# Kernel optimization log

Hardware: AMD Instinct MI355X
Metric: run time of the kernel (lower is better)

The kernel has to match this reference:

```python
import jax, jax.numpy as jnp
import numpy as np

V0, V1, V2 = 8000, 4000, 4096   # diag / proc / med vocab sizes
E = 512                          # emb_dim
T, L = 64, 48                    # visits, codes per visit
FAI = 0.05                       # history-selection threshold
EPS = 1e-5                       # LayerNorm eps (torch default)

def _normalize(adj):
    # GCN.normalize: row-normalize (adj + I)
    adj = adj + np.eye(adj.shape[0], dtype=np.float64)
    rowsum = adj.sum(1)
    r_inv = np.where(rowsum > 0, 1.0 / rowsum, 0.0)
    return (r_inv[:, None] * adj).astype(np.float32)

def setup_inputs() -> dict:
    key = jax.random.key(0)
    ks = iter(jax.random.split(key, 48))
    p = lambda *s: jax.random.normal(next(ks), s, jnp.float32) * 0.02
    rng = np.random.default_rng(0)
    def rand_adj():
        a = rng.random((V2, V2)) < 0.01
        a = (a | a.T).astype(np.float64)
        np.fill_diagonal(a, 0.0)
        return a
    ehr = rand_adj(); ddi = rand_adj()
    return dict(
        diag_codes=jax.random.randint(next(ks), (T, L), 0, V0),
        proc_codes=jax.random.randint(next(ks), (T, L), 0, V1),
        emb0=p(V0, E), emb1=p(V1, E), emb2=p(V2, E),
        gru1_Wih=p(3 * E, E), gru1_Whh=p(3 * E, E), gru1_bih=p(3 * E), gru1_bhh=p(3 * E),
        gru2_Wih=p(3 * E, E), gru2_Whh=p(3 * E, E), gru2_bih=p(3 * E), gru2_bhh=p(3 * E),
        query_W=p(E, 2 * E), query_b=p(E),
        poly_h1_W=p(32, 2 * E), poly_h1_b=p(32), poly_gate_W=p(1, 32), poly_gate_b=p(1),
        cls_W=p(V2, 2 * E), cls_b=p(V2),
        ln_gamma=jnp.ones((E,), jnp.float32), ln_beta=jnp.zeros((E,), jnp.float32),
        ehr_W1=p(V2, E), ehr_b1=p(E), ehr_W2=p(E, E), ehr_b2=p(E),
        ddi_W1=p(V2, E), ddi_b1=p(E), ddi_W2=p(E, E), ddi_b2=p(E),
        inter1=p(1),
        ehr_adj_norm=jnp.asarray(_normalize(ehr)),
        ddi_adj_norm=jnp.asarray(_normalize(ddi)),
        ddi_adj=jnp.asarray(ddi.astype(np.float32)),
    )

def _gru_last(x_seq, mask, Wih, Whh, bih, bhh):
    # torch nn.GRU cell, batch=1; masked-out steps carry h unchanged, which
    # equals running the GRU over only the selected subsequence. Only the
    # final hidden state is needed (original uses output[-1]).
    def step(h, inp):
        x, m = inp
        gi = x @ Wih.T + bih          # [3E]
        gh = h @ Whh.T + bhh
        ir, iz, inn = jnp.split(gi, 3)
        hr, hz, hn = jnp.split(gh, 3)
        r = jax.nn.sigmoid(ir + hr)
        z = jax.nn.sigmoid(iz + hz)
        n = jnp.tanh(inn + r * hn)
        h_new = (1.0 - z) * n + z * h
        return jnp.where(m, h_new, h), None
    h0 = jnp.zeros((Wih.shape[1],), x_seq.dtype)
    h_final, _ = jax.lax.scan(step, h0, (x_seq, mask))
    return h_final

def reference(diag_codes, proc_codes, emb0, emb1, emb2,
              gru1_Wih, gru1_Whh, gru1_bih, gru1_bhh,
              gru2_Wih, gru2_Whh, gru2_bih, gru2_bhh,
              query_W, query_b, poly_h1_W, poly_h1_b, poly_gate_W, poly_gate_b,
              cls_W, cls_b, ln_gamma, ln_beta,
              ehr_W1, ehr_b1, ehr_W2, ehr_b2, ddi_W1, ddi_b1, ddi_W2, ddi_b2,
              inter1, ehr_adj_norm, ddi_adj_norm, ddi_adj):
    i1 = emb0[diag_codes].sum(1)            # [T,E] per-visit sum pooling
    i2 = emb1[proc_codes].sum(1)            # [T,E]
    rep = jnp.concatenate([i1, i2], -1)     # [T,2E] patient representation
    # Aggregation gate for history selection
    hidden = jax.nn.relu(rep @ poly_h1_W.T + poly_h1_b)
    gate = jax.nn.sigmoid(hidden @ poly_gate_W.T + poly_gate_b)[:, 0]  # [T]
    s = jnp.abs(gate[-1] - gate[:-1])
    mask = jnp.concatenate([s <= FAI, jnp.ones((1,), bool)])  # last visit always kept
    h1 = _gru_last(i1, mask, gru1_Wih, gru1_Whh, gru1_bih, gru1_bhh)
    h2 = _gru_last(i2, mask, gru2_Wih, gru2_Whh, gru2_bih, gru2_bhh)
    q_in = jnp.concatenate([h1, h2])                      # [2E]
    query = (jax.nn.relu(q_in) @ query_W.T + query_b)[None, :]  # [1,E]
    def gcn(W1, b1, W2, b2, adj):
        h = jax.nn.relu(adj @ W1 + b1)    # x = I so x@W1 = W1 (dropout eval)
        return adj @ (h @ W2) + b2
    safe = gcn(ehr_W1, ehr_b1, ehr_W2, ehr_b2, ehr_adj_norm) \
         - inter1 * gcn(ddi_W1, ddi_b1, ddi_W2, ddi_b2, ddi_adj_norm)
    drug = safe + emb2                                    # [V2,E]
    kw = jax.nn.softmax(query @ drug.T, -1)               # [1,V2]
    med = kw @ drug                                       # [1,E]
    mu = query.mean(-1, keepdims=True)
    var = ((query - mu) ** 2).mean(-1, keepdims=True)
    ln = (query - mu) / jnp.sqrt(var + EPS) * ln_gamma + ln_beta
    final = jnp.concatenate([ln, med], -1)                # [1,2E]
    result = jax.nn.relu(final) @ cls_W.T + cls_b         # [1,V2]
    neg = jax.nn.sigmoid(result)
    batch_neg = 0.0005 * ((neg.T * neg) * ddi_adj).sum()
    return result, batch_neg
```

## Files before the change

### kernel.cpp

```cpp
#include <hip/hip_runtime.h>
#include <cstdint>
#include <cstddef>

typedef unsigned short u16;
typedef unsigned int   u32;

typedef __bf16 bf16x8 __attribute__((ext_vector_type(8)));
typedef float  f32x4  __attribute__((ext_vector_type(4)));

__device__ __forceinline__ float uAsF(u32 u){ union{u32 u; float f;} c; c.u=u; return c.f; }
__device__ __forceinline__ float b2f(u16 v){ return uAsF(((u32)v)<<16); }
__device__ __forceinline__ u16 f2b(float f){
  union{float f; u32 u;} c; c.f=f; u32 x=c.u;
  u32 r = (x + 0x7fffu + ((x>>16)&1u)) >> 16;
  return (u16)r;
}
__device__ __forceinline__ void unpack8(uint4 p, float* f){
  f[0]=uAsF(p.x<<16); f[1]=uAsF(p.x&0xffff0000u);
  f[2]=uAsF(p.y<<16); f[3]=uAsF(p.y&0xffff0000u);
  f[4]=uAsF(p.z<<16); f[5]=uAsF(p.z&0xffff0000u);
  f[6]=uAsF(p.w<<16); f[7]=uAsF(p.w&0xffff0000u);
}
__device__ __forceinline__ float sigm(float x){ return 1.f/(1.f+__expf(-x)); }

// ... 25 lines not shown
}
__device__ __forceinline__ uint4 ld8p(const void* p, size_t i, int f32){
  if (f32){
    const float4* q = (const float4*)((const float*)p + i);
    float4 a = q[0], b = q[1];
    uint4 r;
    r.x = (u32)f2b(a.x) | ((u32)f2b(a.y)<<16);
    r.y = (u32)f2b(a.z) | ((u32)f2b(a.w)<<16);
    r.z = (u32)f2b(b.x) | ((u32)f2b(b.y)<<16);
    r.w = (u32)f2b(b.z) | ((u32)f2b(b.w)<<16);
    return r;
  }
  return *(const uint4*)((const u16*)p + i);
}

constexpr size_t OFF_I1    = 0;
constexpr size_t OFF_I2    = 0x20000;
constexpr size_t OFF_GI    = 0x40000;
constexpr size_t OFF_GATE  = 0x100000;
constexpr size_t OFF_HBUF  = 0x100800;
constexpr size_t OFF_HFIN  = 0x102800;
constexpr size_t OFF_CTR   = 0x103800;
constexpr size_t OFF_NEGA  = 0x103900;
constexpr size_t OFF_QUERY = 0x104000;
constexpr size_t OFF_SE    = 0x105000;
constexpr size_t OFF_SD    = 0x109000;
constexpr size_t OFF_SEMB  = 0x10D000;
constexpr size_t OFF_KW    = 0x111000;
constexpr size_t OFF_U     = 0x115000;
constexpr size_t OFF_Y     = 0x119000;
constexpr size_t OFF_Z     = 0x11D000;
constexpr size_t OFF_ME    = 0x11D800;
constexpr size_t OFF_MD    = 0x11E000;
constexpr size_t OFF_MEMB  = 0x11E800;
constexpr size_t OFF_FIN   = 0x11F000;
constexpr size_t OFF_NEG   = 0x120000;
constexpr size_t OFF_W1T   = 0x124000;
constexpr size_t OFF_H     = 0x524000;
// ... 7 lines not shown

constexpr size_t OFF_UD    = OFF_GI + 0x0000;
constexpr size_t OFF_Y2    = OFF_GI + 0x4000;
constexpr size_t OFF_Z2    = OFF_GI + 0x8000;
constexpr size_t OFF_WVD   = OFF_GI + 0x8800;
constexpr size_t OFF_WVE   = OFF_GI + 0x9000;

__global__ __launch_bounds__(256) void k_cvt(const void* __restrict__ S, u16* __restrict__ D,
                                             const u16* __restrict__ dt)
{
  int f32 = dprobe(dt);
  size_t i8 = ((size_t)blockIdx.x*256 + threadIdx.x) * 8;
  *(uint4*)(D + i8) = ld8p(S, i8, f32);
}

__global__ __launch_bounds__(256) void k_gather(const int* __restrict__ dc, const int* __restrict__ pc,
    const void* __restrict__ emb0, const void* __restrict__ emb1,
    float* __restrict__ i1, float* __restrict__ i2, const u16* __restrict__ dt)
{
  int f32 = dprobe(dt);
  int t = blockIdx.x;
  int which = blockIdx.y;
  const int* codes = which ? pc : dc;
  const void* emb  = which ? emb1 : emb0;
  float* out       = which ? i2 : i1;
  int e = threadIdx.x;
  float s0=0.f, s1=0.f;
  for (int l=0;l<48;l++){
    int c = codes[t*48+l];
    size_t base = (size_t)c*512;
    s0 += ld1(emb, base+e, f32);
    s1 += ld1(emb, base+e+256, f32);
  }
  out[t*512+e] = s0;
  out[t*512+e+256] = s1;
}

__global__ __launch_bounds__(256) void k_gate(const float* __restrict__ i1, const float* __restrict__ i2,
    const void* __restrict__ phW, const void* __restrict__ phb,
    const void* __restrict__ pgW, const void* __restrict__ pgb,
    float* __restrict__ gate, const u16* __restrict__ dt)
{
  int f32 = dprobe(dt);
  int t = blockIdx.x;
  __shared__ float rep[1024];
  __shared__ float hid[32];
  int tid = threadIdx.x;
  for (int q=0;q<4;q++){
    int k = tid + q*256;
    rep[k] = (k<512) ? i1[t*512+k] : i2[t*512+k-512];
  }
  __syncthreads();
  int w = tid>>6, lane = tid&63;
  for (int jj=0;jj<8;jj++){
    int j = w*8 + jj;
    float s = 0.f;
    for (int k=lane;k<1024;k+=64) s += rep[k]*ld1(phW, (size_t)j*1024+k, f32);
    for (int off=32;off;off>>=1) s += __shfl_down(s, off);
    if (lane==0) hid[j] = fmaxf(s + ld1(phb, j, f32), 0.f);
  }
  __syncthreads();
  if (tid==0){
    float s = 0.f;
    for (int j=0;j<32;j++) s += hid[j]*ld1(pgW, j, f32);
    gate[t] = sigm(s + ld1(pgb, 0, f32));
  }
}

__global__ __launch_bounds__(256) void k_gi(const void* __restrict__ Wih0, const void* __restrict__ Wih1,
    const void* __restrict__ bih0, const void* __restrict__ bih1,
    const float* __restrict__ i1, const float* __restrict__ i2,
    float* __restrict__ gi, const u16* __restrict__ dt)
{
  int f32 = dprobe(dt);
  int g  = blockIdx.y;
  int t0 = blockIdx.x*4;
  const void* W   = g ? Wih1 : Wih0;
  const void* bih = g ? bih1 : bih0;
  const float* x = g ? i2 : i1;
  __shared__ float xl[4*512];
  int tid = threadIdx.x;
  for (int q=0;q<8;q++) xl[tid + q*256] = x[t0*512 + tid + q*256];
  __syncthreads();
  int j = blockIdx.z*256 + tid;
  float b = ld1(bih, j, f32);
  float a0=0.f,a1=0.f,a2=0.f,a3=0.f;
  for (int k=0;k<512;k+=8){
    float f[8]; ld8(W, (size_t)j*512 + k, f32, f);
    #pragma unroll
    for (int xx=0;xx<8;xx++){
      float wv = f[xx];
      a0 += wv*xl[k+xx];
      a1 += wv*xl[512+k+xx];
      a2 += wv*xl[1024+k+xx];
      a3 += wv*xl[1536+k+xx];
    }
  }
  float* og = gi + (size_t)g*64*1536;
  og[(size_t)(t0+0)*1536 + j] = a0 + b;
  og[(size_t)(t0+1)*1536 + j] = a1 + b;
  og[(size_t)(t0+2)*1536 + j] = a2 + b;
  og[(size_t)(t0+3)*1536 + j] = a3 + b;
}

__global__ __launch_bounds__(512, 2) void k_gruf(
    const void* __restrict__ Whh0, const void* __restrict__ Whh1,
    const void* __restrict__ bhh0, const void* __restrict__ bhh1,
    const float* __restrict__ gi, const float* __restrict__ gate,
    u32* __restrict__ hbuf, float* __restrict__ hfin, const u16* __restrict__ dt,
    const void* __restrict__ trS, u16* __restrict__ trD,
    const void* __restrict__ cv0S, u16* __restrict__ cv0D, int nc0,
    const void* __restrict__ cv1S, u16* __restrict__ cv1D, int nc1)
{
  int f32 = dprobe(dt);
  const int tid = threadIdx.x;
  int rb = (int)blockIdx.x - 16;
  if (rb >= 0){
    if (rb < 2048){
      __shared__ u16 tile[32][33];
      int bx = rb & 15, by = rb >> 4;
      int lx = tid & 31, ly = tid >> 5;
      int c = bx*32 + lx;
      #pragma unroll
      for (int i=0;i<2;i++){
        int r = by*32 + ly + i*16;
        size_t idx = (size_t)r*512 + c;
        tile[ly+i*16][lx] = f32 ? f2b(((const float*)trS)[idx]) : ((const u16*)trS)[idx];
      }
      __syncthreads();
      int r2 = by*32 + lx;
      #pragma unroll
      for (int i=0;i<2;i++){
// ... 50 lines not shown
    } else {
      const uint4* src = (const uint4*)((const u16*)Whh + base);
      #pragma unroll
      for (int q=0;q<4;q++){
        uint4 pk = src[q];
        wreg[i*16+q*4+0]=pk.x; wreg[i*16+q*4+1]=pk.y;
        wreg[i*16+q*4+2]=pk.z; wreg[i*16+q*4+3]=pk.w;
      }
    }
  }
  if (tid < 64) gl[tid] = gate[tid];
  h_lds[tid] = 0.f;
  __syncthreads();
  if (tid < 64)
    mask_l[tid] = (tid==63) ? 1 : (fabsf(gl[63] - gl[tid]) <= 0.05f ? 1 : 0);
  __syncthreads();

  int s = 0;
  for (int t=0;t<64;t++){
    if (!mask_l[t]) continue;
    s++;
    const int p = s & 1;
    float acc6[6] = {0.f,0.f,0.f,0.f,0.f,0.f};
    const float2* h2 = ((const float2*)h_lds) + cg*16;
    #pragma unroll
    for (int q=0;q<16;q++){
      float2 hv = h2[q];
      #pragma unroll
      for (int i=0;i<6;i++){
        u32 wp = wreg[i*16+q];
// ... 51 lines not shown
  #pragma unroll
  for (int i=0;i<4;i++){
    int r = blockIdx.y*32 + ly + i*8;
    size_t idx = (size_t)r*C + c;
    tile[ly+i*8][lx] = f32 ? f2b(((const float*)S)[idx]) : ((const u16*)S)[idx];
  }
  __syncthreads();
  int r2 = blockIdx.y*32 + lx;
  #pragma unroll
  for (int i=0;i<4;i++){
    int c2 = blockIdx.x*32 + ly + i*8;
    D[(size_t)c2*R + r2] = tile[lx][ly+i*8];
  }
}

__global__ __launch_bounds__(256)
void k_gemm(const void* __restrict__ A, const u16* __restrict__ Bt,
            const void* __restrict__ bias, u16* __restrict__ C, int K,
            const u16* __restrict__ adt, const u16* __restrict__ bdt)
{
  int af32 = dprobe(adt), bf32 = dprobe(bdt);
  const int m0 = blockIdx.x * 64;
  const int n0 = blockIdx.y * 128;
  const int tid = threadIdx.x;
  const int lane = tid & 63;
  const int wv = tid >> 6;
  const int wr = wv >> 1, wc = wv & 1;
  const int l15 = lane & 15, lq = lane >> 4;

  __shared__ u16 As[2][64*64];
  __shared__ u16 Bs[2][128*64];

  f32x4 acc[2][4];
  #pragma unroll
  for (int i=0;i<2;i++)
    #pragma unroll
    for (int j=0;j<4;j++)
      acc[i][j] = (f32x4){0.f,0.f,0.f,0.f};

  const int srow = tid >> 3;
  const int sc8  = tid & 7;
  const size_t grow_a = (size_t)(m0 + srow) * K + sc8*8;
  const size_t grow_b = (size_t)(n0 + srow) * K + sc8*8;
  const int adst0 = srow*64 + ((sc8 ^ (srow&7))*8);
  const int adst1 = (32+srow)*64 + ((sc8 ^ ((32+srow)&7))*8);
  int bdst[4];
  #pragma unroll
  for (int q=0;q<4;q++){
    int row = q*32 + srow;
    bdst[q] = row*64 + ((sc8 ^ (row&7))*8);
  }

  {
    uint4 va0 = ld8p(A, grow_a, af32);
    uint4 va1 = ld8p(A, grow_a + (size_t)32*K, af32);
    uint4 vb[4];
    #pragma unroll
    for (int q=0;q<4;q++) vb[q] = *(const uint4*)(Bt + grow_b + (size_t)q*32*K);
    *(uint4*)(As[0] + adst0) = va0;
    *(uint4*)(As[0] + adst1) = va1;
    #pragma unroll
    for (int q=0;q<4;q++) *(uint4*)(Bs[0] + bdst[q]) = vb[q];
  }
  __syncthreads();

  for (int k0 = 0; k0 < K; k0 += 64){
    const int cur = (k0 >> 6) & 1;
    const int nxt = 1 - cur;
    uint4 va0, va1, vb[4];
    const bool more = (k0 + 64) < K;
    if (more){
      va0 = ld8p(A, grow_a + k0 + 64, af32);
      va1 = ld8p(A, grow_a + (size_t)32*K + k0 + 64, af32);
      #pragma unroll
      for (int q=0;q<4;q++) vb[q] = *(const uint4*)(Bt + grow_b + (size_t)q*32*K + k0 + 64);
    }
    #pragma unroll
    for (int ks=0; ks<2; ++ks){
      bf16x8 af[2], bfr[4];
      #pragma unroll
      for (int i=0;i<2;i++){
        int ar = wr*32 + i*16 + l15;
        af[i]  = *(const bf16x8*)(As[cur] + ar*64 + (((ks*4+lq) ^ (ar&7))*8));
      }
      #pragma unroll
      for (int j=0;j<4;j++){
        int br = wc*64 + j*16 + l15;
        bfr[j] = *(const bf16x8*)(Bs[cur] + br*64 + (((ks*4+lq) ^ (br&7))*8));
      }
      #pragma unroll
      for (int i=0;i<2;i++)
        #pragma unroll
        for (int j=0;j<4;j++)
          acc[i][j] = __builtin_amdgcn_mfma_f32_16x16x32_bf16(af[i], bfr[j], acc[i][j], 0,0,0);
    }
    if (more){
      *(uint4*)(As[nxt] + adst0) = va0;
      *(uint4*)(As[nxt] + adst1) = va1;
      #pragma unroll
      for (int q=0;q<4;q++) *(uint4*)(Bs[nxt] + bdst[q]) = vb[q];
      __syncthreads();
    }
  }

  #pragma unroll
  for (int i=0;i<2;i++){
    int row = wr*32 + i*16 + lq*4;
    #pragma unroll
    for (int j=0;j<4;j++){
      int col = wc*64 + j*16 + l15;
      int n = n0 + col;
      float bv = ld1(bias, n, bf32);
      #pragma unroll
      for (int r=0;r<4;r++){
        float v = fmaxf(acc[i][j][r] + bv, 0.f);
        C[(size_t)(m0+row+r)*512 + n] = f2b(v);
      }
    }
  }
}

__global__ __launch_bounds__(256) void k_matvec(const void* __restrict__ A, const float* __restrict__ x,
    float* __restrict__ y, int M, int Kc, const u16* __restrict__ dt)
{
  int f32 = dprobe(dt);
  __shared__ float xl[4096];
  int tid = threadIdx.x;
  for (int k=tid; k<Kc; k+=256) xl[k] = x[k];
  __syncthreads();
  int w = tid>>6, lane = tid&63;
  int r0 = blockIdx.x*16 + w*4;
  for (int i=0;i<4;i++){
    int r = r0 + i;
    float s = 0.f;
    for (int k0 = lane*8; k0 < Kc; k0 += 512){
      float f[8]; ld8(A, (size_t)r*Kc + k0, f32, f);
      #pragma unroll
      for (int xx=0;xx<8;xx++) s += f[xx]*xl[k0+xx];
    }
    for (int off=32;off;off>>=1) s += __shfl_down(s, off);
    if (lane==0) y[r] = s;
  }
}

__global__ __launch_bounds__(256) void k_mvp(
    const void* __restrict__ A0, const float* __restrict__ x0, float* __restrict__ y0, const u16* d0,
    const void* __restrict__ A1, const float* __restrict__ x1, float* __restrict__ y1, const u16* d1,
    int Kc, int half)
{
  __shared__ float xl[4096];
  int bx = blockIdx.x, tid = threadIdx.x;
  const void* A; const float* x; float* y; const u16* dtp; int xb;
  if (bx < half){ A=A0; x=x0; y=y0; dtp=d0; xb=bx; }
  else          { A=A1; x=x1; y=y1; dtp=d1; xb=bx-half; }
  int f32 = dprobe(dtp);
  for (int k=tid; k<Kc; k+=256) xl[k] = x[k];
  __syncthreads();
  int w = tid>>6, lane = tid&63;
  int r0 = xb*16 + w*4;
  for (int i=0;i<4;i++){
    int r = r0 + i;
    float s = 0.f;
    for (int k0 = lane*8; k0 < Kc; k0 += 512){
      float f[8]; ld8(A, (size_t)r*Kc + k0, f32, f);
      #pragma unroll
      for (int xx=0;xx<8;xx++) s += f[xx]*xl[k0+xx];
    }
    for (int off=32;off;off>>=1) s += __shfl_down(s, off);
    if (lane==0) y[r] = s;
  }
}

__global__ __launch_bounds__(256) void k_colreduce(const void* __restrict__ A, const float* __restrict__ w,
    float* __restrict__ y, int C, const u16* __restrict__ dt)
{
  int f32 = dprobe(dt);
  __shared__ float wl[256];
  int tid = threadIdx.x;
  int v0 = blockIdx.y*256;
  wl[tid] = w[v0+tid];
  __syncthreads();
  int k = blockIdx.x*256 + tid;
  float acc = 0.f;
  size_t base = (size_t)v0*C + k;
  for (int i=0;i<256;i++) acc += wl[i]*ld1(A, base + (size_t)i*C, f32);
  atomicAdd(&y[k], acc);
}

__global__ __launch_bounds__(256) void k_cr3(
    const void* __restrict__ Ae, const u16* aedt, float* __restrict__ ye,
    const void* __restrict__ Ad, const u16* addt, float* __restrict__ yd,
    const void* __restrict__ E2, const u16* edt, float* __restrict__ ym,
    const float* __restrict__ kw)
{
  __shared__ float wl[256];
  int tid = threadIdx.x, bx = blockIdx.x;
  int v0 = blockIdx.y*256;
  wl[tid] = kw[v0+tid];
  __syncthreads();
  const void* A; float* y; int C, k, f32;
  if (bx < 16){ A=Ae; y=ye; C=4096; k=bx*256+tid; f32=dprobe(aedt); }
  else if (bx < 32){ A=Ad; y=yd; C=4096; k=(bx-16)*256+tid; f32=dprobe(addt); }
  else { A=E2; y=ym; C=512; k=(bx-32)*256+tid; f32=dprobe(edt); }
  float acc = 0.f;
  size_t base = (size_t)v0*C + k;
  for (int i=0;i<256;i++) acc += wl[i]*ld1(A, base + (size_t)i*C, f32);
  atomicAdd(&y[k], acc);
}

__global__ __launch_bounds__(256) void k_crp(
    const void* __restrict__ A0, const float* __restrict__ w0, float* __restrict__ y0, const u16* d0,
    const void* __restrict__ A1, const float* __restrict__ w1, float* __restrict__ y1, const u16* d1,
    int C, int half)
{
  __shared__ float wl[256];
  int tid = threadIdx.x, bx = blockIdx.x;
  int v0 = blockIdx.y*256;
  const void* A; const float* w; float* y; const u16* dtp; int xk;
  if (bx < half){ A=A0; w=w0; y=y0; dtp=d0; xk=bx; }
  else          { A=A1; w=w1; y=y1; dtp=d1; xk=bx-half; }
  int f32 = dprobe(dtp);
  wl[tid] = w[v0+tid];
  __syncthreads();
  int k = xk*256 + tid;
  float acc = 0.f;
  size_t base = (size_t)v0*C + k;
  for (int i=0;i<256;i++) acc += wl[i]*ld1(A, base + (size_t)i*C, f32);
  atomicAdd(&y[k], acc);
}

__global__ void k_zero(float* __restrict__ p, int n){
  int i = blockIdx.x*1024 + threadIdx.x;
  if (i < n) p[i] = 0.f;
}

__global__ __launch_bounds__(256) void k_mv3(
    const void* __restrict__ E2, const void* __restrict__ W2d, const void* __restrict__ W2e,
    const float* __restrict__ query,
    float* __restrict__ s_emb, float* __restrict__ wv_d, float* __restrict__ wv_e,
// ... 158 lines not shown
      float f[4]; ld4(ddi, base + k, f32, f);
      s += f[0]*nl[k] + f[1]*nl[k+1] + f[2]*nl[k+2] + f[3]*nl[k+3];
    }
    for (int off=32;off;off>>=1) s += __shfl_down(s, off);
    if (lane==0) tot += nl[ii]*s;
  }
  if (lane==0) atomicAdd(acc, tot);
  __syncthreads();
  if (tid == 0){
    __threadfence();
    u32 old = atomicAdd(ctr, 1u);
    if (old == (u32)(gridDim.x - 1)){
      float v = 0.0005f * __hip_atomic_load(acc, __ATOMIC_RELAXED, __HIP_MEMORY_SCOPE_AGENT);
      if (f32) ((float*)outv)[4096] = v; else ((u16*)outv)[4096] = f2b(v);
    }
  }
}

__global__ void k_diag(u16* __restrict__ outv, float dv)
{
  int i = blockIdx.x*256 + threadIdx.x;
  if (i <= 4096) outv[i] = (i==0) ? f2b(dv) : (u16)0;
}

extern "C" void kernel_launch(void* const* d_in, const int* in_sizes, int n_in,
                              void* d_out, int out_size, void* d_ws, size_t ws_size,
                              hipStream_t stream)
{
  (void)in_sizes; (void)n_in; (void)out_size;
  const int* diag = (const int*)d_in[0];
// ... 31 lines not shown

  const bool hasHd  = ws_size >= NEED_C2;
  const bool hasAb  = ws_size >= NEED_B;
  const bool hasAb2 = ws_size >= NEED_A;
  const bool mergedTail = hasHd && (hasAb2 || !hasAb);

  char* ws = (char*)d_ws;
  float* i1    = (float*)(ws + OFF_I1);
  float* i2    = (float*)(ws + OFF_I2);
  float* gi    = (float*)(ws + OFF_GI);
  float* gate  = (float*)(ws + OFF_GATE);
  u32*   hbuf  = (u32*)  (ws + OFF_HBUF);
  float* hfin  = (float*)(ws + OFF_HFIN);
  u32*   ctr   = (u32*)  (ws + OFF_CTR);
  float* nega  = (float*)(ws + OFF_NEGA);
  float* query = (float*)(ws + OFF_QUERY);
  float* s_e   = (float*)(ws + OFF_SE);
  float* s_d   = (float*)(ws + OFF_SD);
  float* s_emb = (float*)(ws + OFF_SEMB);
  float* kw    = (float*)(ws + OFF_KW);
  float* u_e   = (float*)(ws + OFF_U);
  float* y     = (float*)(ws + OFF_Y);
  float* z     = (float*)(ws + OFF_Z);
  float* me    = (float*)(ws + OFF_ME);
  float* md    = (float*)(ws + OFF_MD);
  float* memb  = (float*)(ws + OFF_MEMB);
  float* fin   = (float*)(ws + OFF_FIN);
  float* neg   = (float*)(ws + OFF_NEG);
  u16*   W1T   = (u16*)  (ws + OFF_W1T);
  u16*   h     = (u16*)  (ws + OFF_H);
  u16*   h_d   = hasHd ? (u16*)(ws + OFF_HD) : h;
  u16*   AbD   = (u16*)  (ws + OFF_ABD);
  u16*   AbE   = hasAb2 ? (u16*)(ws + OFF_ABE) : AbD;
  float* u_d   = (float*)(ws + OFF_UD);
  float* y2    = (float*)(ws + OFF_Y2);
  float* z2    = (float*)(ws + OFF_Z2);
  float* wv_d  = (float*)(ws + OFF_WVD);
  float* wv_e  = (float*)(ws + OFF_WVE);
  void*  outv  = d_out;

  const void* Ad   = hasAb ? (const void*)AbD : dAdjN;
  const u16*  adt  = hasAb ? (const u16*)nullptr : dt;
  const void* Ae   = hasAb ? (const void*)AbE : eAdj;
  const u16*  aedt = hasAb ? (const u16*)nullptr : dt;

  k_gather<<<dim3(64,2), 256, 0, stream>>>(diag, proc, emb0, emb1, i1, i2, dt);
  k_gate<<<64, 256, 0, stream>>>(i1, i2, phW, phb, pgW, pgb, gate, dt);
  k_gi<<<dim3(16,2,6), 256, 0, stream>>>(g1Wih, g2Wih, g1bih, g2bih, i1, i2, gi, dt);

  {
    int nc0 = hasAb  ? 4096 : 0;
    int nc1 = hasAb2 ? 4096 : 0;
    k_gruf<<<16 + 2048 + nc0 + nc1, 512, 0, stream>>>(
        g1Whh, g2Whh, g1bhh, g2bhh, gi, gate, hbuf, hfin, dt,
        dW1, W1T,
        dAdjN, AbD, nc0,
        eAdj,  AbE, nc1);
  }
  k_query<<<8, 256, 0, stream>>>(hfin, qW, qb, query, dt);
  k_mv3<<<328, 256, 0, stream>>>(emb2, dW2, eW2, query, s_emb, wv_d, wv_e,
                                 y, y2, nega, ctr, dt);

  if (mergedTail){
    k_gemm<<<dim3(64,4), 256, 0, stream>>>(Ad, W1T, db1, h_d, 4096, adt, dt);
    k_transpose<<<dim3(16,128), 256, 0, stream>>>(eW1, W1T, 4096, 512, dt);
    k_gemm<<<dim3(64,4), 256, 0, stream>>>(Ae, W1T, eb1, h, 4096, aedt, dt);
    k_mvp<<<512, 256, 0, stream>>>(h, wv_e, u_e, nullptr, h_d, wv_d, u_d, nullptr, 512, 256);
    k_mvp<<<512, 256, 0, stream>>>(Ae, u_e, s_e, aedt, Ad, u_d, s_d, adt, 4096, 256);
    k_softmax<<<1, 1024, 0, stream>>>(s_e, s_d, s_emb, inter1, kw, dt);
    k_cr3<<<dim3(34,16), 256, 0, stream>>>(Ae, aedt, y, Ad, adt, y2, emb2, dt, memb, kw);
    k_crp<<<dim3(4,16), 256, 0, stream>>>(h, y, z, nullptr, h_d, y2, z2, nullptr, 512, 2);
    k_crp<<<dim3(4,2), 256, 0, stream>>>(eW2, z, me, dt, dW2, z2, md, dt, 512, 2);
  } else {
    k_gemm<<<dim3(64,4), 256, 0, stream>>>(Ad, W1T, db1, h_d, 4096, adt, dt);
    k_matvec<<<256, 256, 0, stream>>>(h_d, wv_d, u_e, 4096, 512, nullptr);
    k_matvec<<<256, 256, 0, stream>>>(Ad, u_e, s_d, 4096, 4096, adt);

    if (hasAb) k_cvt<<<8192, 256, 0, stream>>>(eAdj, AbE, dt);
    k_transpose<<<dim3(16,128), 256, 0, stream>>>(eW1, W1T, 4096, 512, dt);
    k_gemm<<<dim3(64,4), 256, 0, stream>>>(Ae, W1T, eb1, h, 4096, aedt, dt);
    k_matvec<<<256, 256, 0, stream>>>(h, wv_e, u_e, 4096, 512, nullptr);
    k_matvec<<<256, 256, 0, stream>>>(Ae, u_e, s_e, 4096, 4096, aedt);

    k_softmax<<<1, 1024, 0, stream>>>(s_e, s_d, s_emb, inter1, kw, dt);

    k_colreduce<<<dim3(16,16), 256, 0, stream>>>(Ae, kw, y, 4096, aedt);
    k_colreduce<<<dim3(2,16),  256, 0, stream>>>(h,  y,  z, 512,  nullptr);
    k_colreduce<<<dim3(2,2),   256, 0, stream>>>(eW2, z, me, 512, dt);
    k_colreduce<<<dim3(2,16),  256, 0, stream>>>(emb2, kw, memb, 512, dt);

    k_zero<<<5, 1024, 0, stream>>>(y, 4608);
    if (hasAb && !hasAb2) k_cvt<<<8192, 256, 0, stream>>>(dAdjN, AbD, dt);
    if (!hasHd){
      k_transpose<<<dim3(16,128), 256, 0, stream>>>(dW1, W1T, 4096, 512, dt);
      k_gemm<<<dim3(64,4), 256, 0, stream>>>(Ad, W1T, db1, h, 4096, adt, dt);
    }
    k_colreduce<<<dim3(16,16), 256, 0, stream>>>(Ad, kw, y, 4096, adt);
    k_colreduce<<<dim3(2,16),  256, 0, stream>>>(h_d, y, z, 512, nullptr);
    k_colreduce<<<dim3(2,2),   256, 0, stream>>>(dW2, z, md, 512, dt);
  }

  k_ln<<<1, 512, 0, stream>>>(query, me, md, memb, eb2, db2, inter1, lng, lnb, fin, dt);
  k_cls<<<64, 256, 0, stream>>>(fin, clsW, clsb, outv, neg, dt);
  k_negsum<<<128, 256, 0, stream>>>(dAdj, neg, nega, ctr, outv, dt);
}
```

Measured before the change: 1.067 ms.

## Fuse tail into persistent kernel with grid barriers; merge gather/gate and gi into GRU launch

Replaces the chain of about a dozen tail launches (query, matvecs, two GEMMs, softmax, column reductions, layernorm, classifier, negsum) with one persistent 256-block kernel that separates phases using atomic-counter grid barriers. Gather and gate become one kernel, and the input-projection GEMM runs as extra blocks inside the GRU launch, which spin-waits on a counter before starting the recurrence. The goal is to remove launch gaps and small-kernel tails. The cost is spin-barrier overhead, GEMMs limited to 256 resident blocks, and a deadlock risk if not all blocks are co-resident.

```diff
diff --git a/kernel.cpp b/kernel.cpp
--- a/kernel.cpp
+++ b/kernel.cpp
@@ -63,6 +63,18 @@
   return *(const uint4*)((const u16*)p + i);
 }
 
+__device__ __forceinline__ void gbar(u32* cell, u32 n){
+  __syncthreads();
+  if (threadIdx.x == 0){
+    __threadfence();
+    __hip_atomic_fetch_add(cell, 1u, __ATOMIC_RELEASE, __HIP_MEMORY_SCOPE_AGENT);
+    while (__hip_atomic_load(cell, __ATOMIC_ACQUIRE, __HIP_MEMORY_SCOPE_AGENT) < n)
+      __builtin_amdgcn_s_sleep(2);
+    __threadfence();
+  }
+  __syncthreads();
+}
+
 constexpr size_t OFF_I1    = 0;
 constexpr size_t OFF_I2    = 0x20000;
 constexpr size_t OFF_GI    = 0x40000;
@@ -71,6 +83,7 @@
 constexpr size_t OFF_HFIN  = 0x102800;
 constexpr size_t OFF_CTR   = 0x103800;
 constexpr size_t OFF_NEGA  = 0x103900;
+constexpr size_t OFF_BAR   = 0x103A00;
 constexpr size_t OFF_QUERY = 0x104000;
 constexpr size_t OFF_SE    = 0x105000;
 constexpr size_t OFF_SD    = 0x109000;
@@ -108,42 +121,36 @@
   *(uint4*)(D + i8) = ld8p(S, i8, f32);
 }
 
-__global__ __launch_bounds__(256) void k_gather(const int* __restrict__ dc, const int* __restrict__ pc,
+__global__ __launch_bounds__(256) void k_gg(const int* __restrict__ dc, const int* __restrict__ pc,
     const void* __restrict__ emb0, const void* __restrict__ emb1,
-    float* __restrict__ i1, float* __restrict__ i2, const u16* __restrict__ dt)
-{
-  int f32 = dprobe(dt);
-  int t = blockIdx.x;
-  int which = blockIdx.y;
-  const int* codes = which ? pc : dc;
-  const void* emb  = which ? emb1 : emb0;
-  float* out       = which ? i2 : i1;
-  int e = threadIdx.x;
-  float s0=0.f, s1=0.f;
-  for (int l=0;l<48;l++){
-    int c = codes[t*48+l];
-    size_t base = (size_t)c*512;
-    s0 += ld1(emb, base+e, f32);
-    s1 += ld1(emb, base+e+256, f32);
-  }
-  out[t*512+e] = s0;
-  out[t*512+e+256] = s1;
-}
-
-__global__ __launch_bounds__(256) void k_gate(const float* __restrict__ i1, const float* __restrict__ i2,
     const void* __restrict__ phW, const void* __restrict__ phb,
     const void* __restrict__ pgW, const void* __restrict__ pgb,
-    float* __restrict__ gate, const u16* __restrict__ dt)
-{
+    float* __restrict__ i1, float* __restrict__ i2, float* __restrict__ gate,
+    u32* __restrict__ bars, float* __restrict__ nega, const u16* __restrict__ dt)
+{
+  int tid = threadIdx.x;
+  if (blockIdx.x == 64){
+    if (tid < 32) bars[tid] = 0u;
+    if (tid == 32) *nega = 0.f;
+    return;
+  }
   int f32 = dprobe(dt);
   int t = blockIdx.x;
   __shared__ float rep[1024];
   __shared__ float hid[32];
-  int tid = threadIdx.x;
-  for (int q=0;q<4;q++){
-    int k = tid + q*256;
-    rep[k] = (k<512) ? i1[t*512+k] : i2[t*512+k-512];
-  }
+  float s0=0.f, s1=0.f, s2=0.f, s3=0.f;
+  for (int l=0;l<48;l++){
+    int c0 = dc[t*48+l];
+    int c1 = pc[t*48+l];
+    size_t b0 = (size_t)c0*512, b1 = (size_t)c1*512;
+    s0 += ld1(emb0, b0+tid, f32);
+    s1 += ld1(emb0, b0+tid+256, f32);
+    s2 += ld1(emb1, b1+tid, f32);
+    s3 += ld1(emb1, b1+tid+256, f32);
+  }
+  i1[t*512+tid] = s0; i1[t*512+tid+256] = s1;
+  i2[t*512+tid] = s2; i2[t*512+tid+256] = s3;
+  rep[tid] = s0; rep[tid+256] = s1; rep[512+tid] = s2; rep[768+tid] = s3;
   __syncthreads();
   int w = tid>>6, lane = tid&63;
   for (int jj=0;jj<8;jj++){
@@ -161,47 +168,15 @@
   }
 }
 
-__global__ __launch_bounds__(256) void k_gi(const void* __restrict__ Wih0, const void* __restrict__ Wih1,
+__global__ __launch_bounds__(512, 2) void k_gruf2(
+    const void* __restrict__ Whh0, const void* __restrict__ Whh1,
+    const void* __restrict__ bhh0, const void* __restrict__ bhh1,
+    const void* __restrict__ Wih0, const void* __restrict__ Wih1,
     const void* __restrict__ bih0, const void* __restrict__ bih1,
     const float* __restrict__ i1, const float* __restrict__ i2,
-    float* __restrict__ gi, const u16* __restrict__ dt)
-{
-  int f32 = dprobe(dt);
-  int g  = blockIdx.y;
-  int t0 = blockIdx.x*4;
-  const void* W   = g ? Wih1 : Wih0;
-  const void* bih = g ? bih1 : bih0;
-  const float* x = g ? i2 : i1;
-  __shared__ float xl[4*512];
-  int tid = threadIdx.x;
-  for (int q=0;q<8;q++) xl[tid + q*256] = x[t0*512 + tid + q*256];
-  __syncthreads();
-  int j = blockIdx.z*256 + tid;
-  float b = ld1(bih, j, f32);
-  float a0=0.f,a1=0.f,a2=0.f,a3=0.f;
-  for (int k=0;k<512;k+=8){
-    float f[8]; ld8(W, (size_t)j*512 + k, f32, f);
-    #pragma unroll
-    for (int xx=0;xx<8;xx++){
-      float wv = f[xx];
-      a0 += wv*xl[k+xx];
-      a1 += wv*xl[512+k+xx];
-      a2 += wv*xl[1024+k+xx];
-      a3 += wv*xl[1536+k+xx];
-    }
-  }
-  float* og = gi + (size_t)g*64*1536;
-  og[(size_t)(t0+0)*1536 + j] = a0 + b;
-  og[(size_t)(t0+1)*1536 + j] = a1 + b;
-  og[(size_t)(t0+2)*1536 + j] = a2 + b;
-  og[(size_t)(t0+3)*1536 + j] = a3 + b;
-}
-
-__global__ __launch_bounds__(512, 2) void k_gruf(
-    const void* __restrict__ Whh0, const void* __restrict__ Whh1,
-    const void* __restrict__ bhh0, const void* __restrict__ bhh1,
-    const float* __restrict__ gi, const float* __restrict__ gate,
-    u32* __restrict__ hbuf, float* __restrict__ hfin, const u16* __restrict__ dt,
+    float* __restrict__ gi, const float* __restrict__ gate,
+    u32* __restrict__ hbuf, float* __restrict__ hfin,
+    u32* __restrict__ bars, const u16* __restrict__ dt,
     const void* __restrict__ trS, u16* __restrict__ trD,
     const void* __restrict__ cv0S, u16* __restrict__ cv0D, int nc0,
     const void* __restrict__ cv1S, u16* __restrict__ cv1D, int nc1)
@@ -210,6 +185,41 @@
   const int tid = threadIdx.x;
   int rb = (int)blockIdx.x - 16;
   if (rb >= 0){
+    if (rb < 96){
+      __shared__ float xg[2048];
+      int g = (rb>>4)&1, z = rb>>5, t0 = (rb&15)*4;
+      const float* x   = g ? i2 : i1;
+      const void* W    = g ? Wih1 : Wih0;
+      const void* bih  = g ? bih1 : bih0;
+      for (int q=0;q<4;q++) xg[tid + q*512] = x[t0*512 + tid + q*512];
+      __syncthreads();
+      int j = z*512 + tid;
+      float b = ld1(bih, j, f32);
+      float a0=0.f,a1=0.f,a2=0.f,a3=0.f;
+      for (int k=0;k<512;k+=8){
+        float f[8]; ld8(W, (size_t)j*512 + k, f32, f);
+        #pragma unroll
+        for (int xx=0;xx<8;xx++){
+          float wv = f[xx];
+          a0 += wv*xg[k+xx];
+          a1 += wv*xg[512+k+xx];
+          a2 += wv*xg[1024+k+xx];
+          a3 += wv*xg[1536+k+xx];
+        }
+      }
+      float* og = gi + (size_t)g*64*1536;
+      og[(size_t)(t0+0)*1536 + j] = a0 + b;
+      og[(size_t)(t0+1)*1536 + j] = a1 + b;
+      og[(size_t)(t0+2)*1536 + j] = a2 + b;
+      og[(size_t)(t0+3)*1536 + j] = a3 + b;
+      __syncthreads();
+      if (tid == 0){
+        __threadfence();
+        __hip_atomic_fetch_add(&bars[31], 1u, __ATOMIC_RELEASE, __HIP_MEMORY_SCOPE_AGENT);
+      }
+      return;
+    }
+    rb -= 96;
     if (rb < 2048){
       __shared__ u16 tile[32][33];
       int bx = rb & 15, by = rb >> 4;
@@ -290,6 +300,12 @@
   __syncthreads();
   if (tid < 64)
     mask_l[tid] = (tid==63) ? 1 : (fabsf(gl[63] - gl[tid]) <= 0.05f ? 1 : 0);
+  __syncthreads();
+  if (tid == 0){
+    while (__hip_atomic_load(&bars[31], __ATOMIC_ACQUIRE, __HIP_MEMORY_SCOPE_AGENT) < 96u)
+      __builtin_amdgcn_s_sleep(2);
+    __threadfence();
+  }
   __syncthreads();
 
   int s = 0;
@@ -371,22 +387,16 @@
   }
 }
 
-__global__ __launch_bounds__(256)
-void k_gemm(const void* __restrict__ A, const u16* __restrict__ Bt,
-            const void* __restrict__ bias, u16* __restrict__ C, int K,
-            const u16* __restrict__ adt, const u16* __restrict__ bdt)
-{
-  int af32 = dprobe(adt), bf32 = dprobe(bdt);
-  const int m0 = blockIdx.x * 64;
-  const int n0 = blockIdx.y * 128;
-  const int tid = threadIdx.x;
+__device__ __forceinline__ void gemm_body(const void* A, const u16* Bt,
+    const void* bias, u16* C, int af32, int bf32, int task, u16* As, u16* Bs, int tid)
+{
+  const int K = 4096;
+  const int m0 = (task & 63) * 64;
+  const int n0 = (task >> 6) * 128;
   const int lane = tid & 63;
   const int wv = tid >> 6;
   const int wr = wv >> 1, wc = wv & 1;
   const int l15 = lane & 15, lq = lane >> 4;
-
-  __shared__ u16 As[2][64*64];
-  __shared__ u16 Bs[2][128*64];
 
   f32x4 acc[2][4];
   #pragma unroll
@@ -414,10 +424,10 @@
     uint4 vb[4];
     #pragma unroll
     for (int q=0;q<4;q++) vb[q] = *(const uint4*)(Bt + grow_b + (size_t)q*32*K);
-    *(uint4*)(As[0] + adst0) = va0;
-    *(uint4*)(As[0] + adst1) = va1;
+    *(uint4*)(As + adst0) = va0;
+    *(uint4*)(As + adst1) = va1;
     #pragma unroll
-    for (int q=0;q<4;q++) *(uint4*)(Bs[0] + bdst[q]) = vb[q];
+    for (int q=0;q<4;q++) *(uint4*)(Bs + bdst[q]) = vb[q];
   }
   __syncthreads();
 
@@ -432,18 +442,20 @@
       #pragma unroll
       for (int q=0;q<4;q++) vb[q] = *(const uint4*)(Bt + grow_b + (size_t)q*32*K + k0 + 64);
     }
+    u16* Asc = As + cur*4096;
+    u16* Bsc = Bs + cur*8192;
     #pragma unroll
     for (int ks=0; ks<2; ++ks){
       bf16x8 af[2], bfr[4];
       #pragma unroll
       for (int i=0;i<2;i++){
         int ar = wr*32 + i*16 + l15;
-        af[i]  = *(const bf16x8*)(As[cur] + ar*64 + (((ks*4+lq) ^ (ar&7))*8));
+        af[i]  = *(const bf16x8*)(Asc + ar*64 + (((ks*4+lq) ^ (ar&7))*8));
       }
       #pragma unroll
       for (int j=0;j<4;j++){
         int br = wc*64 + j*16 + l15;
-        bfr[j] = *(const bf16x8*)(Bs[cur] + br*64 + (((ks*4+lq) ^ (br&7))*8));
+        bfr[j] = *(const bf16x8*)(Bsc + br*64 + (((ks*4+lq) ^ (br&7))*8));
       }
       #pragma unroll
       for (int i=0;i<2;i++)
@@ -452,10 +464,12 @@
           acc[i][j] = __builtin_amdgcn_mfma_f32_16x16x32_bf16(af[i], bfr[j], acc[i][j], 0,0,0);
     }
     if (more){
-      *(uint4*)(As[nxt] + adst0) = va0;
-      *(uint4*)(As[nxt] + adst1) = va1;
-      #pragma unroll
-      for (int q=0;q<4;q++) *(uint4*)(Bs[nxt] + bdst[q]) = vb[q];
+      u16* Asn = As + nxt*4096;
+      u16* Bsn = Bs + nxt*8192;
+      *(uint4*)(Asn + adst0) = va0;
+      *(uint4*)(Asn + adst1) = va1;
+      #pragma unroll
+      for (int q=0;q<4;q++) *(uint4*)(Bsn + bdst[q]) = vb[q];
       __syncthreads();
     }
   }
@@ -477,6 +491,19 @@
   }
 }
 
+__global__ __launch_bounds__(256)
+void k_gemm(const void* __restrict__ A, const u16* __restrict__ Bt,
+            const void* __restrict__ bias, u16* __restrict__ C, int K,
+            const u16* __restrict__ adt, const u16* __restrict__ bdt)
+{
+  (void)K;
+  __shared__ __attribute__((aligned(16))) char smem[49152];
+  int task = (int)(blockIdx.x + blockIdx.y*64);
+  int t = (int)blockIdx.x | ((int)blockIdx.y << 6);
+  (void)task;
+  gemm_body(A, Bt, bias, C, dprobe(adt), dprobe(bdt), t, (u16*)smem, (u16*)(smem+16384), threadIdx.x);
+}
+
 __global__ __launch_bounds__(256) void k_matvec(const void* __restrict__ A, const float* __restrict__ x,
     float* __restrict__ y, int M, int Kc, const u16* __restrict__ dt)
 {
@@ -500,34 +527,6 @@
   }
 }
 
-__global__ __launch_bounds__(256) void k_mvp(
-    const void* __restrict__ A0, const float* __restrict__ x0, float* __restrict__ y0, const u16* d0,
-    const void* __restrict__ A1, const float* __restrict__ x1, float* __restrict__ y1, const u16* d1,
-    int Kc, int half)
-{
-  __shared__ float xl[4096];
-  int bx = blockIdx.x, tid = threadIdx.x;
-  const void* A; const float* x; float* y; const u16* dtp; int xb;
-  if (bx < half){ A=A0; x=x0; y=y0; dtp=d0; xb=bx; }
-  else          { A=A1; x=x1; y=y1; dtp=d1; xb=bx-half; }
-  int f32 = dprobe(dtp);
-  for (int k=tid; k<Kc; k+=256) xl[k] = x[k];
-  __syncthreads();
-  int w = tid>>6, lane = tid&63;
-  int r0 = xb*16 + w*4;
-  for (int i=0;i<4;i++){
-    int r = r0 + i;
-    float s = 0.f;
-    for (int k0 = lane*8; k0 < Kc; k0 += 512){
-      float f[8]; ld8(A, (size_t)r*Kc + k0, f32, f);
-      #pragma unroll
-      for (int xx=0;xx<8;xx++) s += f[xx]*xl[k0+xx];
-    }
-    for (int off=32;off;off>>=1) s += __shfl_down(s, off);
-    if (lane==0) y[r] = s;
-  }
-}
-
 __global__ __launch_bounds__(256) void k_colreduce(const void* __restrict__ A, const float* __restrict__ w,
     float* __restrict__ y, int C, const u16* __restrict__ dt)
 {
@@ -538,48 +537,6 @@
   wl[tid] = w[v0+tid];
   __syncthreads();
   int k = blockIdx.x*256 + tid;
-  float acc = 0.f;
-  size_t base = (size_t)v0*C + k;
-  for (int i=0;i<256;i++) acc += wl[i]*ld1(A, base + (size_t)i*C, f32);
-  atomicAdd(&y[k], acc);
-}
-
-__global__ __launch_bounds__(256) void k_cr3(
-    const void* __restrict__ Ae, const u16* aedt, float* __restrict__ ye,
-    const void* __restrict__ Ad, const u16* addt, float* __restrict__ yd,
-    const void* __restrict__ E2, const u16* edt, float* __restrict__ ym,
-    const float* __restrict__ kw)
-{
-  __shared__ float wl[256];
-  int tid = threadIdx.x, bx = blockIdx.x;
-  int v0 = blockIdx.y*256;
-  wl[tid] = kw[v0+tid];
-  __syncthreads();
-  const void* A; float* y; int C, k, f32;
-  if (bx < 16){ A=Ae; y=ye; C=4096; k=bx*256+tid; f32=dprobe(aedt); }
-  else if (bx < 32){ A=Ad; y=yd; C=4096; k=(bx-16)*256+tid; f32=dprobe(addt); }
-  else { A=E2; y=ym; C=512; k=(bx-32)*256+tid; f32=dprobe(edt); }
-  float acc = 0.f;
-  size_t base = (size_t)v0*C + k;
-  for (int i=0;i<256;i++) acc += wl[i]*ld1(A, base + (size_t)i*C, f32);
-  atomicAdd(&y[k], acc);
-}
-
-__global__ __launch_bounds__(256) void k_crp(
-    const void* __restrict__ A0, const float* __restrict__ w0, float* __restrict__ y0, const u16* d0,
-    const void* __restrict__ A1, const float* __restrict__ w1, float* __restrict__ y1, const u16* d1,
-    int C, int half)
-{
-  __shared__ float wl[256];
-  int tid = threadIdx.x, bx = blockIdx.x;
-  int v0 = blockIdx.y*256;
-  const void* A; const float* w; float* y; const u16* dtp; int xk;
-  if (bx < half){ A=A0; w=w0; y=y0; dtp=d0; xk=bx; }
-  else          { A=A1; w=w1; y=y1; dtp=d1; xk=bx-half; }
-  int f32 = dprobe(dtp);
-  wl[tid] = w[v0+tid];
-  __syncthreads();
-  int k = xk*256 + tid;
   float acc = 0.f;
   size_t base = (size_t)v0*C + k;
   for (int i=0;i<256;i++) acc += wl[i]*ld1(A, base + (size_t)i*C, f32);
@@ -768,6 +725,317 @@
       float v = 0.0005f * __hip_atomic_load(acc, __ATOMIC_RELAXED, __HIP_MEMORY_SCOPE_AGENT);
       if (f32) ((float*)outv)[4096] = v; else ((u16*)outv)[4096] = f2b(v);
     }
+  }
+}
+
+__global__ __launch_bounds__(256) void k_tail(
+    const float* hfin, const void* qW, const void* qb, float* query,
+    const void* emb2, const void* dW2, const void* eW2,
+    float* s_emb, float* wv_d, float* wv_e,
+    const void* Ad, const u16* adt, const void* Ae, const u16* aedt,
+    u16* W1T, const void* db1, const void* eb1, u16* h_d, u16* h_,
+    const void* eW1,
+    float* u_e, float* u_d, float* s_e, float* s_d,
+    const void* inter1, float* kw,
+    float* y, float* y2, float* z, float* z2,
+    float* me, float* mdp, float* memb,
+    const void* eb2, const void* db2, const void* gam, const void* bet, float* fin,
+    const void* clsW, const void* clsb, void* outv, float* neg,
+    const void* ddi, float* nega, u32* bars, const u16* dt)
+{
+  __shared__ __attribute__((aligned(16))) char smem[49152];
+  float* fsm = (float*)smem;
+  const int tid = threadIdx.x;
+  const int bid = blockIdx.x;
+  const u32 nb = gridDim.x;
+  const int f32 = dprobe(dt);
+  const int af  = dprobe(adt);
+  const int ef  = dprobe(aedt);
+  const int w = tid>>6, lane = tid&63;
+
+  if (bid < 8){
+    float* qin = fsm;
+    for (int q=0;q<4;q++){ int k=tid+q*256; qin[k] = fmaxf(hfin[k], 0.f); }
+    __syncthreads();
+    int row0 = bid*64 + w*16;
+    for (int i=0;i<16;i++){
+      int rr = row0 + i;
+      float s = 0.f;
+      for (int k=lane;k<1024;k+=64) s += qin[k]*ld1(qW, (size_t)rr*1024+k, f32);
+      for (int off=32;off;off>>=1) s += __shfl_down(s, off);
+      if (lane==0) query[rr] = s + ld1(qb, rr, f32);
+    }
+  }
+  gbar(&bars[0], nb);
+
+  {
+    float* xl = fsm;
+    for (int k=tid;k<512;k+=256) xl[k] = query[k];
+    __syncthreads();
+    for (int t=bid; t<327; t+=nb){
+      if (t < 320){
+        const void* A; float* yy; int xb;
+        if (t < 256){ A=emb2; yy=s_emb; xb=t; }
+        else if (t < 288){ A=dW2; yy=wv_d; xb=t-256; }
+        else { A=eW2; yy=wv_e; xb=t-288; }
+        int r0 = xb*16 + w*4;
+        for (int i=0;i<4;i++){
+          int r = r0 + i;
+          float s = 0.f;
+          int k0 = lane*8;
+          float f[8]; ld8(A, (size_t)r*512 + k0, f32, f);
+          #pragma unroll
+          for (int xx=0;xx<8;xx++) s += f[xx]*xl[k0+xx];
+          for (int off=32;off;off>>=1) s += __shfl_down(s, off);
+          if (lane==0) yy[r] = s;
+        }
+      } else if (t < 324){
+        int rb = t - 320;
+        #pragma unroll
+        for (int q=0;q<6;q++){ int i = rb*1536 + q*256 + tid; if (i < 6144) y[i] = 0.f; }
+      } else {
+        int c = t - 324;
+        #pragma unroll
+        for (int q=0;q<6;q++){ int i = c*1536 + q*256 + tid; if (i < 4608) y2[i] = 0.f; }
+      }
+    }
+  }
+  gbar(&bars[1], nb);
+
+  gemm_body(Ad, W1T, db1, h_d, af, f32, bid, (u16*)smem, (u16*)(smem+16384), tid);
+  gbar(&bars[2], nb);
+
+  {
+    u16* tl = (u16*)smem;
+    int lx = tid & 31, ly = tid >> 5;
+    for (int t=bid; t<2048; t+=nb){
+      int bx = t & 15, by = t >> 4;
+      int c = bx*32 + lx;
+      #pragma unroll
+      for (int i=0;i<4;i++){
+        int r = by*32 + ly + i*8;
+        size_t idx = (size_t)r*512 + c;
+        tl[(ly+i*8)*33 + lx] = f32 ? f2b(((const float*)eW1)[idx]) : ((const u16*)eW1)[idx];
+      }
+      __syncthreads();
+      int r2 = by*32 + lx;
+      #pragma unroll
+      for (int i=0;i<4;i++){
+        int c2 = bx*32 + ly + i*8;
+        W1T[(size_t)c2*4096 + r2] = tl[lx*33 + ly+i*8];
+      }
+      __syncthreads();
+    }
+  }
+  gbar(&bars[3], nb);
+
+  gemm_body(Ae, W1T, eb1, h_, ef, f32, bid, (u16*)smem, (u16*)(smem+16384), tid);
+  gbar(&bars[4], nb);
+
+  {
+    float* xl = fsm;
+    for (int t=bid; t<512; t+=nb){
+      const u16* A; const float* x; float* yy; int xb;
+      if (t < 256){ A=h_; x=wv_e; yy=u_e; xb=t; }
+      else { A=h_d; x=wv_d; yy=u_d; xb=t-256; }
+      for (int k=tid;k<512;k+=256) xl[k] = x[k];
+      __syncthreads();
+      int r0 = xb*16 + w*4;
+      for (int i=0;i<4;i++){
+        int r = r0 + i;
+        float s = 0.f;
+        int k0 = lane*8;
+        float f[8]; ld8(A, (size_t)r*512 + k0, 0, f);
+        #pragma unroll
+        for (int xx=0;xx<8;xx++) s += f[xx]*xl[k0+xx];
+        for (int off=32;off;off>>=1) s += __shfl_down(s, off);
+        if (lane==0) yy[r] = s;
+      }
+      __syncthreads();
+    }
+  }
+  gbar(&bars[5], nb);
+
+  {
+    float* xl = fsm;
+    for (int t=bid; t<512; t+=nb){
+      const void* A; const float* x; float* yy; int xb, ff;
+      if (t < 256){ A=Ae; x=u_e; yy=s_e; xb=t; ff=ef; }
+      else { A=Ad; x=u_d; yy=s_d; xb=t-256; ff=af; }
+      for (int k=tid;k<4096;k+=256) xl[k] = x[k];
+      __syncthreads();
+      int r0 = xb*16 + w*4;
+      for (int i=0;i<4;i++){
+        int r = r0 + i;
+        float s = 0.f;
+        for (int k0=lane*8; k0<4096; k0+=512){
+          float f[8]; ld8(A, (size_t)r*4096 + k0, ff, f);
+          #pragma unroll
+          for (int xx=0;xx<8;xx++) s += f[xx]*xl[k0+xx];
+        }
+        for (int off=32;off;off>>=1) s += __shfl_down(s, off);
+        if (lane==0) yy[r] = s;
+      }
+      __syncthreads();
+    }
+  }
+  gbar(&bars[6], nb);
+
+  if (bid == 0){
+    float* red = fsm;
+    float it1 = ld1(inter1, 0, f32);
+    float v[16]; float m = -1e30f;
+    #pragma unroll
+    for (int q=0;q<16;q++){
+      int i = tid + q*256;
+      v[q] = s_e[i] - it1*s_d[i] + s_emb[i];
+      m = fmaxf(m, v[q]);
+    }
+    red[tid] = m; __syncthreads();
+    for (int s=128;s;s>>=1){ if (tid<s) red[tid] = fmaxf(red[tid], red[tid+s]); __syncthreads(); }
+    m = red[0]; __syncthreads();
+    float sum = 0.f;
+    #pragma unroll
+    for (int q=0;q<16;q++){ v[q] = __expf(v[q]-m); sum += v[q]; }
+    red[tid] = sum; __syncthreads();
+    for (int s=128;s;s>>=1){ if (tid<s) red[tid] += red[tid+s]; __syncthreads(); }
+    float inv = 1.f/red[0];
+    #pragma unroll
+    for (int q=0;q<16;q++) kw[tid + q*256] = v[q]*inv;
+  }
+  gbar(&bars[7], nb);
+
+  {
+    float* wl = fsm;
+    for (int t=bid; t<544; t+=nb){
+      int bx = t % 34, by = t / 34;
+      int v0 = by*256;
+      wl[tid] = kw[v0+tid];
+      __syncthreads();
+      const void* A; float* yy; int C, k, ff;
+      if (bx < 16){ A=Ae; yy=y; C=4096; k=bx*256+tid; ff=ef; }
+      else if (bx < 32){ A=Ad; yy=y2; C=4096; k=(bx-16)*256+tid; ff=af; }
+      else { A=emb2; yy=memb; C=512; k=(bx-32)*256+tid; ff=f32; }
+      float acc = 0.f;
+      size_t base = (size_t)v0*C + k;
+      for (int i=0;i<256;i++) acc += wl[i]*ld1(A, base + (size_t)i*C, ff);
+      atomicAdd(&yy[k], acc);
+      __syncthreads();
+    }
+  }
+  gbar(&bars[8], nb);
+
+  {
+    float* wl = fsm;
+    for (int t=bid; t<64; t+=nb){
+      int bx = t & 3, by = t >> 2;
+      int v0 = by*256;
+      const u16* A; const float* ww; float* yy; int xk;
+      if (bx < 2){ A=h_; ww=y; yy=z; xk=bx; }
+      else { A=h_d; ww=y2; yy=z2; xk=bx-2; }
+      wl[tid] = ww[v0+tid];
+      __syncthreads();
+      int k = xk*256 + tid;
+      float acc = 0.f;
+      size_t base = (size_t)v0*512 + k;
+      for (int i=0;i<256;i++) acc += wl[i]*b2f(A[base + (size_t)i*512]);
+      atomicAdd(&yy[k], acc);
+      __syncthreads();
+    }
+  }
+  gbar(&bars[9], nb);
+
+  {
+    float* wl = fsm;
+    for (int t=bid; t<8; t+=nb){
+      int bx = t & 3, by = t >> 2;
+      int v0 = by*256;
+      const void* A; const float* ww; float* yy; int xk;
+      if (bx < 2){ A=eW2; ww=z; yy=me; xk=bx; }
+      else { A=dW2; ww=z2; yy=mdp; xk=bx-2; }
+      wl[tid] = ww[v0+tid];
+      __syncthreads();
+      int k = xk*256 + tid;
+      float acc = 0.f;
+      size_t base = (size_t)v0*512 + k;
+      for (int i=0;i<256;i++) acc += wl[i]*ld1(A, base + (size_t)i*512, f32);
+      atomicAdd(&yy[k], acc);
+      __syncthreads();
+    }
+  }
+  gbar(&bars[10], nb);
+
+  if (bid == 0){
+    float* red = fsm;
+    float q0 = query[tid], q1 = query[tid+256];
+    red[tid] = q0 + q1; __syncthreads();
+    for (int s=128;s;s>>=1){ if (tid<s) red[tid] += red[tid+s]; __syncthreads(); }
+    float mu = red[0]/512.f; __syncthreads();
+    float d0 = q0 - mu, d1 = q1 - mu;
+    red[tid] = d0*d0 + d1*d1; __syncthreads();
+    for (int s=128;s;s>>=1){ if (tid<s) red[tid] += red[tid+s]; __syncthreads(); }
+    float rstd = rsqrtf(red[0]/512.f + 1e-5f);
+    float it1 = ld1(inter1, 0, f32);
+    int e0 = tid, e1 = tid + 256;
+    float ln0 = d0*rstd*ld1(gam,e0,f32) + ld1(bet,e0,f32);
+    float ln1 = d1*rstd*ld1(gam,e1,f32) + ld1(bet,e1,f32);
+    float mv0 = (me[e0] + ld1(eb2,e0,f32)) - it1*(mdp[e0] + ld1(db2,e0,f32)) + memb[e0];
+    float mv1 = (me[e1] + ld1(eb2,e1,f32)) - it1*(mdp[e1] + ld1(db2,e1,f32)) + memb[e1];
+    fin[e0] = fmaxf(ln0, 0.f);
+    fin[e1] = fmaxf(ln1, 0.f);
+    fin[512+e0] = fmaxf(mv0, 0.f);
+    fin[512+e1] = fmaxf(mv1, 0.f);
+  }
+  gbar(&bars[11], nb);
+
+  if (bid < 64){
+    float* fl = fsm;
+    for (int q=0;q<4;q++) fl[tid+q*256] = fin[tid+q*256];
+    __syncthreads();
+    int v0b = bid*64 + w*16;
+    for (int i=0;i<16;i++){
+      int v = v0b + i;
+      float f[16];
+      ld8(clsW, (size_t)v*1024 + lane*16, f32, f);
+      ld8(clsW, (size_t)v*1024 + lane*16 + 8, f32, f+8);
+      const float* q16 = fl + lane*16;
+      float s = 0.f;
+      #pragma unroll
+      for (int x=0;x<16;x++) s += f[x]*q16[x];
+      for (int off=32;off;off>>=1) s += __shfl_down(s, off);
+      if (lane==0){
+        s += ld1(clsb, v, f32);
+        if (f32) ((float*)outv)[v] = s; else ((u16*)outv)[v] = f2b(s);
+        neg[v] = sigm(s);
+      }
+    }
+  }
+  gbar(&bars[12], nb);
+
+  if (bid < 128){
+    float* nl = fsm;
+    for (int q=0;q<16;q++) nl[tid+q*256] = neg[tid+q*256];
+    __syncthreads();
+    int i0 = bid*32 + w*8;
+    float tot = 0.f;
+    for (int i=0;i<8;i++){
+      int ii = i0 + i;
+      size_t base = (size_t)ii*4096;
+      float s = 0.f;
+      for (int step=0; step<16; step++){
+        int k = lane*4 + step*256;
+        float f[4]; ld4(ddi, base + k, f32, f);
+        s += f[0]*nl[k] + f[1]*nl[k+1] + f[2]*nl[k+2] + f[3]*nl[k+3];
+      }
+      for (int off=32;off;off>>=1) s += __shfl_down(s, off);
+      if (lane==0) tot += nl[ii]*s;
+    }
+    if (lane==0) atomicAdd(nega, tot);
+  }
+  gbar(&bars[13], nb);
+  if (bid == 0 && tid == 0){
+    float v = 0.0005f * __hip_atomic_load(nega, __ATOMIC_RELAXED, __HIP_MEMORY_SCOPE_AGENT);
+    if (f32) ((float*)outv)[4096] = v; else ((u16*)outv)[4096] = f2b(v);
   }
 }
 
@@ -829,6 +1097,7 @@
   float* hfin  = (float*)(ws + OFF_HFIN);
   u32*   ctr   = (u32*)  (ws + OFF_CTR);
   float* nega  = (float*)(ws + OFF_NEGA);
+  u32*   bars  = (u32*)  (ws + OFF_BAR);
   float* query = (float*)(ws + OFF_QUERY);
   float* s_e   = (float*)(ws + OFF_SE);
   float* s_d   = (float*)(ws + OFF_SD);
@@ -859,34 +1128,39 @@
   const void* Ae   = hasAb ? (const void*)AbE : eAdj;
   const u16*  aedt = hasAb ? (const u16*)nullptr : dt;
 
-  k_gather<<<dim3(64,2), 256, 0, stream>>>(diag, proc, emb0, emb1, i1, i2, dt);
-  k_gate<<<64, 256, 0, stream>>>(i1, i2, phW, phb, pgW, pgb, gate, dt);
-  k_gi<<<dim3(16,2,6), 256, 0, stream>>>(g1Wih, g2Wih, g1bih, g2bih, i1, i2, gi, dt);
+  k_gg<<<65, 256, 0, stream>>>(diag, proc, emb0, emb1, phW, phb, pgW, pgb,
+                               i1, i2, gate, bars, nega, dt);
 
   {
     int nc0 = hasAb  ? 4096 : 0;
     int nc1 = hasAb2 ? 4096 : 0;
-    k_gruf<<<16 + 2048 + nc0 + nc1, 512, 0, stream>>>(
-        g1Whh, g2Whh, g1bhh, g2bhh, gi, gate, hbuf, hfin, dt,
+    k_gruf2<<<16 + 96 + 2048 + nc0 + nc1, 512, 0, stream>>>(
+        g1Whh, g2Whh, g1bhh, g2bhh,
+        g1Wih, g2Wih, g1bih, g2bih,
+        i1, i2, gi, gate, hbuf, hfin, bars, dt,
         dW1, W1T,
         dAdjN, AbD, nc0,
         eAdj,  AbE, nc1);
   }
-  k_query<<<8, 256, 0, stream>>>(hfin, qW, qb, query, dt);
-  k_mv3<<<328, 256, 0, stream>>>(emb2, dW2, eW2, query, s_emb, wv_d, wv_e,
-                                 y, y2, nega, ctr, dt);
 
   if (mergedTail){
-    k_gemm<<<dim3(64,4), 256, 0, stream>>>(Ad, W1T, db1, h_d, 4096, adt, dt);
-    k_transpose<<<dim3(16,128), 256, 0, stream>>>(eW1, W1T, 4096, 512, dt);
-    k_gemm<<<dim3(64,4), 256, 0, stream>>>(Ae, W1T, eb1, h, 4096, aedt, dt);
-    k_mvp<<<512, 256, 0, stream>>>(h, wv_e, u_e, nullptr, h_d, wv_d, u_d, nullptr, 512, 256);
-    k_mvp<<<512, 256, 0, stream>>>(Ae, u_e, s_e, aedt, Ad, u_d, s_d, adt, 4096, 256);
-    k_softmax<<<1, 1024, 0, stream>>>(s_e, s_d, s_emb, inter1, kw, dt);
-    k_cr3<<<dim3(34,16), 256, 0, stream>>>(Ae, aedt, y, Ad, adt, y2, emb2, dt, memb, kw);
-    k_crp<<<dim3(4,16), 256, 0, stream>>>(h, y, z, nullptr, h_d, y2, z2, nullptr, 512, 2);
-    k_crp<<<dim3(4,2), 256, 0, stream>>>(eW2, z, me, dt, dW2, z2, md, dt, 512, 2);
+    k_tail<<<256, 256, 0, stream>>>(
+        hfin, qW, qb, query,
+        emb2, dW2, eW2,
+        s_emb, wv_d, wv_e,
+        Ad, adt, Ae, aedt,
+        W1T, db1, eb1, h_d, h,
+        eW1,
+        u_e, u_d, s_e, s_d,
+        inter1, kw,
+        y, y2, z, z2, me, md, memb,
+        eb2, db2, lng, lnb, fin,
+        clsW, clsb, outv, neg,
+        dAdj, nega, bars, dt);
   } else {
+    k_query<<<8, 256, 0, stream>>>(hfin, qW, qb, query, dt);
+    k_mv3<<<328, 256, 0, stream>>>(emb2, dW2, eW2, query, s_emb, wv_d, wv_e,
+                                   y, y2, nega, ctr, dt);
     k_gemm<<<dim3(64,4), 256, 0, stream>>>(Ad, W1T, db1, h_d, 4096, adt, dt);
     k_matvec<<<256, 256, 0, stream>>>(h_d, wv_d, u_e, 4096, 512, nullptr);
     k_matvec<<<256, 256, 0, stream>>>(Ad, u_e, s_d, 4096, 4096, adt);
@@ -913,9 +1187,9 @@
     k_colreduce<<<dim3(16,16), 256, 0, stream>>>(Ad, kw, y, 4096, adt);
     k_colreduce<<<dim3(2,16),  256, 0, stream>>>(h_d, y, z, 512, nullptr);
     k_colreduce<<<dim3(2,2),   256, 0, stream>>>(dW2, z, md, 512, dt);
-  }
-
-  k_ln<<<1, 512, 0, stream>>>(query, me, md, memb, eb2, db2, inter1, lng, lnb, fin, dt);
-  k_cls<<<64, 256, 0, stream>>>(fin, clsW, clsb, outv, neg, dt);
-  k_negsum<<<128, 256, 0, stream>>>(dAdj, neg, nega, ctr, outv, dt);
-}
+
+    k_ln<<<1, 512, 0, stream>>>(query, me, md, memb, eb2, db2, inter1, lng, lnb, fin, dt);
+    k_cls<<<64, 256, 0, stream>>>(fin, clsW, clsb, outv, neg, dt);
+    k_negsum<<<128, 256, 0, stream>>>(dAdj, neg, nega, ctr, outv, dt);
+  }
+}
```

After: 2.326 ms. +118.1%, slower.
